# Kernel optimization log

Hardware: AMD Instinct MI355X
Metric: run time of the kernel (lower is better)

Reference implementation:

```python
import jax, jax.numpy as jnp
import numpy as np

N_NODES = 100000
N_EDGES = 1250000
IN_CH = 128
OUT_CH = 64


def setup_inputs() -> dict:
    key = jax.random.key(0)
    k1, k2, k3, k4 = jax.random.split(key, 4)
    x = jax.random.normal(k1, (N_NODES, IN_CH), dtype=jnp.float32)
    edge_index = jax.random.randint(k2, (2, N_EDGES), 0, N_NODES, dtype=jnp.int64)
    edge_weight = jax.random.uniform(k3, (N_EDGES,), dtype=jnp.float32)
    # Xavier-uniform weight, zero bias (as in reset_parameters)
    limit = float(np.sqrt(6.0 / (IN_CH + OUT_CH)))
    W = jax.random.uniform(k4, (IN_CH, OUT_CH), dtype=jnp.float32, minval=-limit, maxval=limit)
    b = jnp.zeros((OUT_CH,), dtype=jnp.float32)
    return {"x": x, "edge_index": edge_index, "edge_weight": edge_weight, "W": W, "b": b}


def reference(x, edge_index, edge_weight, W, b):
    # Dense transform: [N, in] @ [in, out] -> [N, out]
    h = jnp.matmul(x, W)
    row, col = edge_index[0], edge_index[1]
    n = h.shape[0]
    # Weighted in-degree via scatter-add on destination (row)
    deg = jnp.zeros((n,), dtype=h.dtype).at[row].add(edge_weight)
    # deg^-0.5 with inf (deg==0) replaced by 0
    deg_inv_sqrt = jnp.where(deg == 0, jnp.zeros_like(deg), deg ** -0.5)
    norm = deg_inv_sqrt[row] * deg_inv_sqrt[col]  # [E]
    # Gather source features, normalize, scatter-add to destinations
    out = jnp.zeros_like(h).at[row].add(h[col] * norm[:, None])
    return out + b
```

## Files before the change

### kernel.cpp

```cpp
#include <hip/hip_runtime.h>

#define N_NODES 100000
#define N_EDGES 1250000
#define IN_CH 128
#define OUT_CH 64

#define BIN_NODES 256
#define NBINS 391
#define BINCAP_DEF 4096
#define NB1 512
#define CH1 ((N_EDGES + NB1 - 1) / NB1)
#define MAXU ((CH1 + 255) / 256)
#define CURS_STRIDE 16

typedef __attribute__((ext_vector_type(8))) short short8;
typedef __attribute__((ext_vector_type(4))) float f32x4;

__device__ inline unsigned int f2bf(float f) {
    unsigned int u = __float_as_uint(f);
    unsigned int r = ((u >> 16) & 1u) + 0x7FFFu;
    return (u + r) >> 16;
}
__device__ inline float bf_lo(unsigned int p) { return __uint_as_float(p << 16); }
__device__ inline float bf_hi(unsigned int p) { return __uint_as_float(p & 0xFFFF0000u); }

__global__ __launch_bounds__(256) void wbconv_kernel(const float* __restrict__ W,
                                                     unsigned int* __restrict__ Wb,
                                                     int* __restrict__ cursor,
                                                     int bincap) {
    int g = blockIdx.x * 256 + threadIdx.x;
    if (g < NBINS) cursor[g * CURS_STRIDE] = g * bincap;

    int c = g >> 8;
    int t = (g >> 6) & 3;
    int l = g & 63;
    int q = l >> 4, r15 = l & 15;
    unsigned int o[4];
#pragma unroll
    for (int jj = 0; jj < 4; ++jj) {
        float f0 = W[(c * 32 + q * 8 + 2 * jj)     * OUT_CH + t * 16 + r15];
        float f1 = W[(c * 32 + q * 8 + 2 * jj + 1) * OUT_CH + t * 16 + r15];
        o[jj] = f2bf(f0) | (f2bf(f1) << 16);
    }
    *(uint4*)(Wb + (size_t)g * 4) = make_uint4(o[0], o[1], o[2], o[3]);
}

__global__ __launch_bounds__(256) void bin1_kernel(const int* __restrict__ ei,
                                                   const float* __restrict__ ew,
                                                   int* __restrict__ cursor,
                                                   int2* __restrict__ brec,
                                                   int bincap) {
    __shared__ int hist[NBINS];
    __shared__ int base[NBINS];
    __shared__ int rank[NBINS];
    const int t = threadIdx.x;
    for (int i = t; i < NBINS; i += 256) { hist[i] = 0; rank[i] = 0; }
    __syncthreads();

    const int e0 = blockIdx.x * CH1;
    const int e1 = (e0 + CH1 < N_EDGES) ? e0 + CH1 : N_EDGES;

    int rowv[MAXU], colv[MAXU];
    float wv[MAXU];
#pragma unroll
    for (int u = 0; u < MAXU; ++u) {
        int e = e0 + t + u * 256;
        bool ok = e < e1;
        rowv[u] = ok ? ei[e] : -1;
        colv[u] = ok ? ei[N_EDGES + e] : 0;
        wv[u]   = ok ? ew[e] : 0.0f;
        if (ok) atomicAdd(&hist[rowv[u] >> 8], 1);
    }
    __syncthreads();

    for (int i = t; i < NBINS; i += 256)
        if (hist[i] > 0) base[i] = atomicAdd(&cursor[i * CURS_STRIDE], hist[i]);
    __syncthreads();

#pragma unroll
    for (int u = 0; u < MAXU; ++u) {
        if (rowv[u] >= 0) {
            int b = rowv[u] >> 8;
            int rk = atomicAdd(&rank[b], 1);
            int idx = base[b] + rk;
            if (idx < (b + 1) * bincap)
                brec[idx] = make_int2(((rowv[u] & 255) << 17) | colv[u],
                                      __float_as_int(wv[u]));
        }
    }
}

__global__ __launch_bounds__(256) void bin2_kernel(const int* __restrict__ cursor,
                                                   const int2* __restrict__ brec,
                                                   int* __restrict__ srt,
                                                   int* __restrict__ cnt_g,
                                                   int* __restrict__ start_g,
                                                   float* __restrict__ dis_g,
                                                   int bincap) {
    __shared__ int   cnt[256];
    __shared__ int   scan[256];
    __shared__ int   slot[256];
    __shared__ float deg[256];
    const int t = threadIdx.x;
    const int b = blockIdx.x;
    cnt[t] = 0; slot[t] = 0; deg[t] = 0.0f;
    __syncthreads();

    const int rbase = b * bincap;
    int m = cursor[b * CURS_STRIDE] - rbase;
    if (m > bincap) m = bincap;

    for (int j = t; j < m; j += 256) {
        int2 rec = brec[rbase + j];
        int rl = rec.x >> 17;
        atomicAdd(&cnt[rl], 1);
        atomicAdd(&deg[rl], __int_as_float(rec.y));
    }
    __syncthreads();

    int v = cnt[t];
    scan[t] = v;
    __syncthreads();
#pragma unroll
    for (int off = 1; off < 256; off <<= 1) {
        int a = 0;
        if (t >= off) a = scan[t - off];
        __syncthreads();
        if (t >= off) scan[t] += a;
        __syncthreads();
    }
    int mystart = scan[t] - v;

    int node = b * BIN_NODES + t;
    if (node < N_NODES) {
        cnt_g[node]   = v;
        start_g[node] = rbase + mystart;
        float d = deg[t];
        dis_g[node] = (d == 0.0f) ? 0.0f : (1.0f / sqrtf(d));
    }
    __syncthreads();
    scan[t] = mystart;
    __syncthreads();

    for (int j = t; j < m; j += 256) {
        int2 rec = brec[rbase + j];
        int rl  = rec.x >> 17;
        int col = rec.x & 0x1FFFF;
        int sc = atomicAdd(&slot[rl], 1);
        srt[rbase + scan[rl] + sc] = col;
    }
}

__global__ __launch_bounds__(256) void gemm_kernel(const float* __restrict__ x,
                                                   const unsigned int* __restrict__ Wb,
                                                   const float* __restrict__ dis,
                                                   unsigned int* __restrict__ hs) {
    const int tid  = threadIdx.x;
    const int w    = tid >> 6;
    const int lane = tid & 63;
    const int q    = lane >> 4, r15 = lane & 15;
    const int node = blockIdx.x * 64 + w * 16 + r15;
    const int nl   = (node < N_NODES) ? node : N_NODES - 1;
    const float* xrow = x + (size_t)nl * IN_CH;

    f32x4 acc[4];
#pragma unroll
    for (int t = 0; t < 4; ++t) acc[t] = (f32x4){0.f, 0.f, 0.f, 0.f};

#pragma unroll
    for (int c = 0; c < 4; ++c) {
        float4 xa = *(const float4*)(xrow + c * 32 + q * 8);
        float4 xb = *(const float4*)(xrow + c * 32 + q * 8 + 4);
        short8 bfrag;
        bfrag[0] = (short)f2bf(xa.x); bfrag[1] = (short)f2bf(xa.y);
        bfrag[2] = (short)f2bf(xa.z); bfrag[3] = (short)f2bf(xa.w);
        bfrag[4] = (short)f2bf(xb.x); bfrag[5] = (short)f2bf(xb.y);
        bfrag[6] = (short)f2bf(xb.z); bfrag[7] = (short)f2bf(xb.w);
#pragma unroll
        for (int t = 0; t < 4; ++t) {
            short8 afrag = *(const short8*)(Wb + (size_t)((c * 4 + t) * 64 + lane) * 4);
            acc[t] = __builtin_amdgcn_mfma_f32_16x16x32_bf16(afrag, bfrag, acc[t], 0, 0, 0);
        }
    }

    if (node < N_NODES) {
        float di = dis[node];
#pragma unroll
        for (int t = 0; t < 4; ++t) {
            unsigned int p0 = f2bf(acc[t][0] * di) | (f2bf(acc[t][1] * di) << 16);
            unsigned int p1 = f2bf(acc[t][2] * di) | (f2bf(acc[t][3] * di) << 16);
            *(uint2*)(hs + (size_t)node * 32 + t * 8 + q * 2) = make_uint2(p0, p1);
        }
    }
}

__global__ __launch_bounds__(256) void gather_kernel(const int* __restrict__ start,
                                                     const int* __restrict__ cnt,
                                                     const int* __restrict__ srt,
                                                     const float* __restrict__ dis,
                                                     const uint2* __restrict__ hs,
                                                     const float* __restrict__ b,
                                                     float* __restrict__ out) {
    int lane = threadIdx.x & 63;
    int qtr  = lane >> 4;
    int l    = lane & 15;
    int i = (blockIdx.x * 4 + (threadIdx.x >> 6)) * 4 + qtr;
    if (i >= N_NODES) return;

    int s = start[i];
    int n = cnt[i];
    float a0 = 0.f, a1 = 0.f, a2 = 0.f, a3 = 0.f;
    int j = 0;
    for (; j + 1 < n; j += 2) {
        int c0 = srt[s + j];
        int c1 = srt[s + j + 1];
        uint2 p0 = hs[(size_t)c0 * 16 + l];
        uint2 p1 = hs[(size_t)c1 * 16 + l];
        a0 += bf_lo(p0.x); a1 += bf_hi(p0.x); a2 += bf_lo(p0.y); a3 += bf_hi(p0.y);
        a0 += bf_lo(p1.x); a1 += bf_hi(p1.x); a2 += bf_lo(p1.y); a3 += bf_hi(p1.y);
    }
    if (j < n) {
        int c0 = srt[s + j];
        uint2 p0 = hs[(size_t)c0 * 16 + l];
        a0 += bf_lo(p0.x); a1 += bf_hi(p0.x); a2 += bf_lo(p0.y); a3 += bf_hi(p0.y);
    }
    float di = dis[i];
    float4 bb = *(const float4*)&b[4 * l];
    float4 o = make_float4(a0 * di + bb.x, a1 * di + bb.y,
                           a2 * di + bb.z, a3 * di + bb.w);
    *(float4*)&out[(size_t)i * OUT_CH + 4 * l] = o;
}

extern "C" void kernel_launch(void* const* d_in, const int* in_sizes, int n_in,
                              void* d_out, int out_size, void* d_ws, size_t ws_size,
                              hipStream_t stream) {
    const float* x  = (const float*)d_in[0];
    const int*   ei = (const int*)d_in[1];
    const float* ew = (const float*)d_in[2];
    const float* W  = (const float*)d_in[3];
    const float* b  = (const float*)d_in[4];
    float* out = (float*)d_out;

    unsigned int* hs = (unsigned int*)d_ws;
    unsigned int* Wb = hs + (size_t)N_NODES * 32;
    int*   cursor  = (int*)(Wb + 4096);
    int*   cnt_g   = cursor + NBINS * CURS_STRIDE;
    int*   start_g = cnt_g + N_NODES;
    float* dis     = (float*)(start_g + N_NODES);
    int2*  brec    = (int2*)(dis + N_NODES);
    size_t used = (size_t)N_NODES * 32 + 4096 + (size_t)NBINS * CURS_STRIDE
                + 3 * (size_t)N_NODES;
    size_t rem  = (ws_size / 4 > used) ? ws_size / 4 - used : 0;
    int bincap  = (int)(rem / (3 * (size_t)NBINS));
    if (bincap > BINCAP_DEF) bincap = BINCAP_DEF;
    int* srt = (int*)(brec + (size_t)NBINS * bincap);

    wbconv_kernel<<<4, 256, 0, stream>>>(W, Wb, cursor, bincap);
    bin1_kernel<<<NB1, 256, 0, stream>>>(ei, ew, cursor, brec, bincap);
    bin2_kernel<<<NBINS, 256, 0, stream>>>(cursor, brec, srt, cnt_g, start_g, dis, bincap);
    gemm_kernel<<<(N_NODES + 63) / 64, 256, 0, stream>>>(x, Wb, dis, hs);
    gather_kernel<<<(N_NODES + 15) / 16, 256, 0, stream>>>(start_g, cnt_g, srt, dis,
                                                           (const uint2*)hs, b, out);
}
```

Measured before the change: 187.2 us.

## Widen gather loads to 16 bytes, use wavefront-shuffle scan, enlarge bin1 blocks

The gather kernel now gives each node 8 lanes that each load a uint4 (8 bf16 values) instead of 16 lanes loading uint2, so twice as many nodes are handled per wavefront and fewer, wider memory requests are issued. In bin2, the shared-memory Hillis-Steele scan with many barriers is replaced by a shuffle-based scan within each wavefront plus a small cross-wave sum. bin1 switches to 256 blocks of 512 threads. These changes aim to cut gather memory transaction count and scan synchronisation overhead, at the cost of more registers per lane in the gather and fewer, larger bin1 blocks.

```diff
diff --git a/kernel.cpp b/kernel.cpp
--- a/kernel.cpp
+++ b/kernel.cpp
@@ -8,9 +8,10 @@
 #define BIN_NODES 256
 #define NBINS 391
 #define BINCAP_DEF 4096
-#define NB1 512
+#define NB1 256
+#define B1T 512
 #define CH1 ((N_EDGES + NB1 - 1) / NB1)
-#define MAXU ((CH1 + 255) / 256)
+#define MAXU ((CH1 + B1T - 1) / B1T)
 #define CURS_STRIDE 16
 
 typedef __attribute__((ext_vector_type(8))) short short8;
@@ -45,7 +46,7 @@
     *(uint4*)(Wb + (size_t)g * 4) = make_uint4(o[0], o[1], o[2], o[3]);
 }
 
-__global__ __launch_bounds__(256) void bin1_kernel(const int* __restrict__ ei,
+__global__ __launch_bounds__(B1T) void bin1_kernel(const int* __restrict__ ei,
                                                    const float* __restrict__ ew,
                                                    int* __restrict__ cursor,
                                                    int2* __restrict__ brec,
@@ -54,7 +55,7 @@
     __shared__ int base[NBINS];
     __shared__ int rank[NBINS];
     const int t = threadIdx.x;
-    for (int i = t; i < NBINS; i += 256) { hist[i] = 0; rank[i] = 0; }
+    for (int i = t; i < NBINS; i += B1T) { hist[i] = 0; rank[i] = 0; }
     __syncthreads();
 
     const int e0 = blockIdx.x * CH1;
@@ -64,7 +65,7 @@
     float wv[MAXU];
 #pragma unroll
     for (int u = 0; u < MAXU; ++u) {
-        int e = e0 + t + u * 256;
+        int e = e0 + t + u * B1T;
         bool ok = e < e1;
         rowv[u] = ok ? ei[e] : -1;
         colv[u] = ok ? ei[N_EDGES + e] : 0;
@@ -73,7 +74,7 @@
     }
     __syncthreads();
 
-    for (int i = t; i < NBINS; i += 256)
+    for (int i = t; i < NBINS; i += B1T)
         if (hist[i] > 0) base[i] = atomicAdd(&cursor[i * CURS_STRIDE], hist[i]);
     __syncthreads();
 
@@ -101,6 +102,7 @@
     __shared__ int   scan[256];
     __shared__ int   slot[256];
     __shared__ float deg[256];
+    __shared__ int   wsum[4];
     const int t = threadIdx.x;
     const int b = blockIdx.x;
     cnt[t] = 0; slot[t] = 0; deg[t] = 0.0f;
@@ -119,17 +121,20 @@
     __syncthreads();
 
     int v = cnt[t];
-    scan[t] = v;
-    __syncthreads();
-#pragma unroll
-    for (int off = 1; off < 256; off <<= 1) {
-        int a = 0;
-        if (t >= off) a = scan[t - off];
-        __syncthreads();
-        if (t >= off) scan[t] += a;
-        __syncthreads();
-    }
-    int mystart = scan[t] - v;
+    int x = v;
+    int lane = t & 63;
+#pragma unroll
+    for (int off = 1; off < 64; off <<= 1) {
+        int y = __shfl_up(x, off, 64);
+        if (lane >= off) x += y;
+    }
+    if (lane == 63) wsum[t >> 6] = x;
+    __syncthreads();
+    int wbase = 0;
+#pragma unroll
+    for (int k = 0; k < 4; ++k)
+        if (k < (t >> 6)) wbase += wsum[k];
+    int mystart = wbase + x - v;
 
     int node = b * BIN_NODES + t;
     if (node < N_NODES) {
@@ -138,7 +143,6 @@
         float d = deg[t];
         dis_g[node] = (d == 0.0f) ? 0.0f : (1.0f / sqrtf(d));
     }
-    __syncthreads();
     scan[t] = mystart;
     __syncthreads();
 
@@ -198,37 +202,43 @@
                                                      const int* __restrict__ cnt,
                                                      const int* __restrict__ srt,
                                                      const float* __restrict__ dis,
-                                                     const uint2* __restrict__ hs,
+                                                     const uint4* __restrict__ hs,
                                                      const float* __restrict__ b,
                                                      float* __restrict__ out) {
     int lane = threadIdx.x & 63;
-    int qtr  = lane >> 4;
-    int l    = lane & 15;
-    int i = (blockIdx.x * 4 + (threadIdx.x >> 6)) * 4 + qtr;
+    int sub  = lane >> 3;
+    int l    = lane & 7;
+    int i = (blockIdx.x * 4 + (threadIdx.x >> 6)) * 8 + sub;
     if (i >= N_NODES) return;
 
     int s = start[i];
     int n = cnt[i];
     float a0 = 0.f, a1 = 0.f, a2 = 0.f, a3 = 0.f;
+    float a4 = 0.f, a5 = 0.f, a6 = 0.f, a7 = 0.f;
     int j = 0;
     for (; j + 1 < n; j += 2) {
         int c0 = srt[s + j];
         int c1 = srt[s + j + 1];
-        uint2 p0 = hs[(size_t)c0 * 16 + l];
-        uint2 p1 = hs[(size_t)c1 * 16 + l];
+        uint4 p0 = hs[(size_t)c0 * 8 + l];
+        uint4 p1 = hs[(size_t)c1 * 8 + l];
         a0 += bf_lo(p0.x); a1 += bf_hi(p0.x); a2 += bf_lo(p0.y); a3 += bf_hi(p0.y);
+        a4 += bf_lo(p0.z); a5 += bf_hi(p0.z); a6 += bf_lo(p0.w); a7 += bf_hi(p0.w);
         a0 += bf_lo(p1.x); a1 += bf_hi(p1.x); a2 += bf_lo(p1.y); a3 += bf_hi(p1.y);
+        a4 += bf_lo(p1.z); a5 += bf_hi(p1.z); a6 += bf_lo(p1.w); a7 += bf_hi(p1.w);
     }
     if (j < n) {
         int c0 = srt[s + j];
-        uint2 p0 = hs[(size_t)c0 * 16 + l];
+        uint4 p0 = hs[(size_t)c0 * 8 + l];
         a0 += bf_lo(p0.x); a1 += bf_hi(p0.x); a2 += bf_lo(p0.y); a3 += bf_hi(p0.y);
+        a4 += bf_lo(p0.z); a5 += bf_hi(p0.z); a6 += bf_lo(p0.w); a7 += bf_hi(p0.w);
     }
     float di = dis[i];
-    float4 bb = *(const float4*)&b[4 * l];
-    float4 o = make_float4(a0 * di + bb.x, a1 * di + bb.y,
-                           a2 * di + bb.z, a3 * di + bb.w);
-    *(float4*)&out[(size_t)i * OUT_CH + 4 * l] = o;
+    float4 b0 = *(const float4*)&b[8 * l];
+    float4 b1 = *(const float4*)&b[8 * l + 4];
+    float4 o0 = make_float4(a0 * di + b0.x, a1 * di + b0.y, a2 * di + b0.z, a3 * di + b0.w);
+    float4 o1 = make_float4(a4 * di + b1.x, a5 * di + b1.y, a6 * di + b1.z, a7 * di + b1.w);
+    *(float4*)&out[(size_t)i * OUT_CH + 8 * l]     = o0;
+    *(float4*)&out[(size_t)i * OUT_CH + 8 * l + 4] = o1;
 }
 
 extern "C" void kernel_launch(void* const* d_in, const int* in_sizes, int n_in,
@@ -256,9 +266,9 @@
     int* srt = (int*)(brec + (size_t)NBINS * bincap);
 
     wbconv_kernel<<<4, 256, 0, stream>>>(W, Wb, cursor, bincap);
-    bin1_kernel<<<NB1, 256, 0, stream>>>(ei, ew, cursor, brec, bincap);
+    bin1_kernel<<<NB1, B1T, 0, stream>>>(ei, ew, cursor, brec, bincap);
     bin2_kernel<<<NBINS, 256, 0, stream>>>(cursor, brec, srt, cnt_g, start_g, dis, bincap);
     gemm_kernel<<<(N_NODES + 63) / 64, 256, 0, stream>>>(x, Wb, dis, hs);
-    gather_kernel<<<(N_NODES + 15) / 16, 256, 0, stream>>>(start_g, cnt_g, srt, dis,
-                                                           (const uint2*)hs, b, out);
-}
+    gather_kernel<<<(N_NODES + 31) / 32, 256, 0, stream>>>(start_g, cnt_g, srt, dis,
+                                                           (const uint4*)hs, b, out);
+}
```

New measurement: 172.4 us. -7.9%, faster.
